# Optimization experiments

Measured on AMD Instinct MI355X. Metric: run time of the kernel, lower is better.

## Reference

```python
import jax, jax.numpy as jnp
import numpy as np

B, S, H = 16, 1024, 4
QD, KD, VD = 128, 256, 256


def setup_inputs() -> dict:
    key = jax.random.key(0)
    ks = jax.random.split(key, 12)
    s = 0.02
    return {
        "query": jax.random.normal(ks[0], (B, S, QD), jnp.float32),
        "key": jax.random.normal(ks[1], (B, S, KD), jnp.float32),
        "value": jax.random.normal(ks[2], (B, S, VD), jnp.float32),
        "Wq": jax.random.normal(ks[3], (QD, KD * H), jnp.float32) * s,
        "bq": jnp.zeros((KD * H,), jnp.float32),
        "Wk": jax.random.normal(ks[4], (KD, KD * H), jnp.float32) * s,
        "bk": jnp.zeros((KD * H,), jnp.float32),
        "Wv": jax.random.normal(ks[5], (VD, VD * H), jnp.float32) * s,
        "bv": jnp.zeros((VD * H,), jnp.float32),
        "Wo": jax.random.normal(ks[6], (VD * H, 8 * VD), jnp.float32) * s,
        "bo": jnp.zeros((8 * VD,), jnp.float32),
        "W1": jax.random.normal(ks[7], (8 * VD, 128), jnp.float32) * s,
        "b1": jnp.zeros((128,), jnp.float32),
        "random_len": S,
    }


def reference(query, key, value, Wq, bq, Wk, bk, Wv, bv, Wo, bo, W1, b1, random_len):
    b = query.shape[0]
    # flat view [B, S, H*D] -> [B, H, S, D], exactly matching torch .view semantics
    tq = (query @ Wq + bq).reshape(b, H, -1, KD)
    tk = (key @ Wk + bk).reshape(b, H, -1, KD)
    tv = (value @ Wv + bv).reshape(b, H, -1, VD)
    # NOTE: original has NO 1/sqrt(d) scaling
    scores = jnp.einsum("bhqd,bhkd->bhqk", tq, tk)  # [B,H,S,S]
    attn = jax.nn.softmax(scores, axis=-1)
    attended = jnp.einsum("bhqk,bhkd->bhqd", attn, tv)  # [B,H,S,VD]
    attended = attended.reshape(b, -1, VD * H)  # [B,S,H*VD]
    out = attended @ Wo + bo  # [B,S,2048]
    out = out.mean(axis=1)  # [B,2048]
    out = out @ W1 + b1  # [B,128]
    return out, attn
```

## Files before the change

kernel.cpp:

```cpp
#include <hip/hip_runtime.h>
#include <hip/hip_bf16.h>

typedef _Float16 half_t;
typedef _Float16 half8 __attribute__((ext_vector_type(8)));
typedef _Float16 half4v __attribute__((ext_vector_type(4)));
typedef float floatx4 __attribute__((ext_vector_type(4)));

__global__ __launch_bounds__(256) void wtrans_kernel(const float* __restrict__ W,
                                                     half_t* __restrict__ Wt, int K, int N) {
  __shared__ float sm[32][33];
  int n0 = blockIdx.x * 32, k0 = blockIdx.y * 32;
  int x = threadIdx.x & 31, y0 = threadIdx.x >> 5;
#pragma unroll
  for (int yy = 0; yy < 4; ++yy) {
    int y = y0 + yy * 8;
    sm[y][x] = W[(size_t)(k0 + y) * N + n0 + x];
  }
  __syncthreads();
#pragma unroll
  for (int yy = 0; yy < 4; ++yy) {
    int y = y0 + yy * 8;
    Wt[(size_t)(n0 + y) * K + k0 + x] = (half_t)sm[x][y];
  }
}

template <bool AF32, bool BIAS>
__global__ __launch_bounds__(256) void gemm_nt(
    const float* __restrict__ Af, const half_t* __restrict__ Ah,
    const half_t* __restrict__ Bt, const float* __restrict__ bias,
    half_t* __restrict__ C, int K, int ldc,
    size_t aStrideZ, size_t bStrideZ, size_t cStrideZ) {
  __shared__ half_t sA[128 * 32];
  __shared__ half_t sB[128 * 32];
  const int t = threadIdx.x;
  const int m0 = blockIdx.x * 128;
  const int n0 = blockIdx.y * 128;
  const int z = blockIdx.z;
  const half_t* Bz = Bt + bStrideZ * (size_t)z;
  const int w = t >> 6, lane = t & 63;
  const int wm = w & 1, wn = w >> 1;
  const int lr = lane & 15, lk = lane >> 4;
  const int srow = t >> 2, sg = t & 3;

  floatx4 acc[4][4] = {};

  for (int k0 = 0; k0 < K; k0 += 32) {
    __syncthreads();
#pragma unroll
    for (int rep = 0; rep < 2; ++rep) {
      int row = srow + rep * 64;
      int goff = (sg ^ ((row >> 1) & 3)) * 8;
      half8 hv;
      if constexpr (AF32) {
        const float* p = Af + (size_t)(m0 + row) * K + k0 + sg * 8;
        float4 f0 = *(const float4*)p;
        float4 f1 = *(const float4*)(p + 4);
        hv[0] = (half_t)f0.x; hv[1] = (half_t)f0.y;
        hv[2] = (half_t)f0.z; hv[3] = (half_t)f0.w;
        hv[4] = (half_t)f1.x; hv[5] = (half_t)f1.y;
        hv[6] = (half_t)f1.z; hv[7] = (half_t)f1.w;
      } else {
        const half_t* p = Ah + aStrideZ * (size_t)z + (size_t)(m0 + row) * K + k0 + sg * 8;
        hv = *(const half8*)p;
      }
      *(half8*)&sA[row * 32 + goff] = hv;
      const half_t* q = Bz + (size_t)(n0 + row) * K + k0 + sg * 8;
      *(half8*)&sB[row * 32 + goff] = *(const half8*)q;
    }
    __syncthreads();
    half8 af[4], bf[4];
#pragma unroll
    for (int mt = 0; mt < 4; ++mt) {
      int row = wm * 64 + mt * 16 + lr;
      af[mt] = *(const half8*)&sA[row * 32 + ((lk ^ ((row >> 1) & 3)) * 8)];
    }
#pragma unroll
    for (int nt = 0; nt < 4; ++nt) {
      int row = wn * 64 + nt * 16 + lr;
      bf[nt] = *(const half8*)&sB[row * 32 + ((lk ^ ((row >> 1) & 3)) * 8)];
    }
#pragma unroll
    for (int mt = 0; mt < 4; ++mt)
#pragma unroll
      for (int nt = 0; nt < 4; ++nt)
        acc[mt][nt] = __builtin_amdgcn_mfma_f32_16x16x32_f16(bf[nt], af[mt], acc[mt][nt], 0, 0, 0);
  }

  half_t* Cz = C + cStrideZ * (size_t)z;
#pragma unroll
  for (int mt = 0; mt < 4; ++mt) {
    int m = m0 + wm * 64 + mt * 16 + lr;
#pragma unroll
    for (int nt = 0; nt < 4; ++nt) {
      int nb = n0 + wn * 64 + nt * 16 + lk * 4;
      floatx4 a = acc[mt][nt];
      half4v h;
      if constexpr (BIAS) {
        float4 bv = *(const float4*)&bias[nb];
        h[0] = (half_t)(a[0] + bv.x); h[1] = (half_t)(a[1] + bv.y);
        h[2] = (half_t)(a[2] + bv.z); h[3] = (half_t)(a[3] + bv.w);
      } else {
        h[0] = (half_t)a[0]; h[1] = (half_t)a[1];
        h[2] = (half_t)a[2]; h[3] = (half_t)a[3];
      }
      *(half4v*)&Cz[(size_t)m * ldc + nb] = h;
    }
  }
}

__global__ __launch_bounds__(256) void softcs_kernel(float* __restrict__ attn,
                                                     float* __restrict__ cs) {
  int bh = blockIdx.x, slice = blockIdx.y;
  int t = threadIdx.x;
  int w = t >> 6, lane = t & 63;
  float csacc[16];
#pragma unroll
  for (int j = 0; j < 16; ++j) csacc[j] = 0.0f;

  for (int i = 0; i < 16; ++i) {
    int q = slice * 64 + i * 4 + w;
    float* rowp = attn + ((size_t)bh * 1024 + q) * 1024;
    const half_t* sh = (const half_t*)rowp;
    float ex[16];
    float s = 0.0f;
#pragma unroll
    for (int c = 0; c < 4; ++c) {
      half4v h = *(const half4v*)(sh + c * 256 + lane * 4);
#pragma unroll
      for (int j = 0; j < 4; ++j) {
        float e = __expf((float)h[j]);
        ex[c * 4 + j] = e;
        s += e;
      }
    }
#pragma unroll
    for (int off = 1; off < 64; off <<= 1) s += __shfl_xor(s, off);
    float rl = 1.0f / s;
#pragma unroll
    for (int c = 0; c < 4; ++c) {
      float4 o;
      o.x = ex[c * 4 + 0] * rl; o.y = ex[c * 4 + 1] * rl;
      o.z = ex[c * 4 + 2] * rl; o.w = ex[c * 4 + 3] * rl;
      *(float4*)(rowp + c * 256 + lane * 4) = o;
      csacc[c * 4 + 0] += o.x; csacc[c * 4 + 1] += o.y;
      csacc[c * 4 + 2] += o.z; csacc[c * 4 + 3] += o.w;
    }
  }
  float* csp = cs + (size_t)bh * 4096 + (size_t)w * 1024 + lane * 4;
#pragma unroll
  for (int c = 0; c < 4; ++c)
#pragma unroll
    for (int j = 0; j < 4; ++j)
      atomicAdd(csp + c * 256 + j, csacc[c * 4 + j]);
}

__global__ __launch_bounds__(256) void abar_kernel(const float* __restrict__ cs,
                                                   const half_t* __restrict__ Tv,
                                                   float* __restrict__ abar) {
  int b = blockIdx.x, r = blockIdx.y, kc = blockIdx.z;
  int d = threadIdx.x;
  __shared__ float scs[4][128];
  for (int idx = d; idx < 512; idx += 256) {
    int h = idx >> 7, k = idx & 127;
    scs[h][k] = cs[(size_t)(b * 4 + h) * 4096 + (size_t)r * 1024 + kc * 128 + k];
  }
  __syncthreads();
  float acc = 0.0f;
  for (int h = 0; h < 4; ++h) {
    const half_t* tv = Tv + (size_t)(b * 4 + h) * 262144 + (size_t)kc * 32768 + d;
#pragma unroll 4
    for (int k = 0; k < 128; ++k)
      acc += scs[h][k] * (float)tv[(size_t)k * 256];
  }
  atomicAdd(&abar[b * 1024 + r * 256 + d], acc * (1.0f / 1024.0f));
}

__global__ __launch_bounds__(256) void bcomb_kernel(const float* __restrict__ bo,
                                                    const float* __restrict__ W1,
                                                    const float* __restrict__ b1,
                                                    float* __restrict__ bcomb) {
  int t = threadIdx.x;
  int j = t & 127, h = t >> 7;
  float acc = 0.0f;
  for (int k = h * 1024; k < h * 1024 + 1024; ++k)
    acc += bo[k] * W1[(size_t)k * 128 + j];
  __shared__ float sm[2][128];
  sm[h][j] = acc;
  __syncthreads();
  if (t < 128) bcomb[t] = sm[0][t] + sm[1][t] + b1[t];
}

__global__ __launch_bounds__(256) void final2_kernel(const float* __restrict__ abar,
                                                     const half_t* __restrict__ Wcomb,
                                                     const float* __restrict__ bcomb,
                                                     float* __restrict__ out) {
  int b = blockIdx.x, t = threadIdx.x;
  int j = t & 127, h = t >> 7;
  __shared__ float sa[1024];
  __shared__ float sm[2][128];
  for (int i = t; i < 1024; i += 256) sa[i] = abar[(size_t)b * 1024 + i];
  __syncthreads();
  float acc = 0.0f;
  for (int c = h * 512; c < h * 512 + 512; ++c)
    acc += sa[c] * (float)Wcomb[(size_t)c * 128 + j];
  sm[h][j] = acc;
  __syncthreads();
  if (t < 128) out[(size_t)b * 128 + t] = sm[0][t] + sm[1][t] + bcomb[t];
}

extern "C" void kernel_launch(void* const* d_in, const int* in_sizes, int n_in,
                              void* d_out, int out_size, void* d_ws, size_t ws_size,
                              hipStream_t stream) {
  const float* query = (const float*)d_in[0];
  const float* key   = (const float*)d_in[1];
  const float* value = (const float*)d_in[2];
  const float* Wq = (const float*)d_in[3];
  const float* bq = (const float*)d_in[4];
  const float* Wk = (const float*)d_in[5];
  const float* bk = (const float*)d_in[6];
  const float* Wv = (const float*)d_in[7];
  const float* bv = (const float*)d_in[8];
  const float* Wo = (const float*)d_in[9];
  const float* bo = (const float*)d_in[10];
  const float* W1 = (const float*)d_in[11];
  const float* b1 = (const float*)d_in[12];

  char* ws = (char*)d_ws;
  half_t* Tq   = (half_t*)(ws + 0);
  half_t* Tk   = (half_t*)(ws + 33554432);
  half_t* Tv   = (half_t*)(ws + 67108864);
  float*  cs   = (float*)(ws + 100663296);
  float*  abar = (float*)(ws + 101711872);
  half_t* Wqt  = (half_t*)(ws + 101777408);
  half_t* Wkt  = (half_t*)(ws + 102039552);
  half_t* Wvt  = (half_t*)(ws + 102563840);
  half_t* W1t   = (half_t*)(ws + 0);
  half_t* Wcomb = (half_t*)(ws + 524288);
  float*  bcomb = (float*)(ws + 786432);

  float* out  = (float*)d_out;
  float* attn = out + 2048;

  hipMemsetAsync(cs, 0, 1048576 + 65536, stream);

  wtrans_kernel<<<dim3(32, 4), 256, 0, stream>>>(Wq, Wqt, 128, 1024);
  wtrans_kernel<<<dim3(32, 8), 256, 0, stream>>>(Wk, Wkt, 256, 1024);
  wtrans_kernel<<<dim3(32, 8), 256, 0, stream>>>(Wv, Wvt, 256, 1024);

  gemm_nt<true, true><<<dim3(128, 8, 1), 256, 0, stream>>>(query, nullptr, Wqt, bq, Tq, 128, 1024, 0, 0, 0);
  gemm_nt<true, true><<<dim3(128, 8, 1), 256, 0, stream>>>(key,   nullptr, Wkt, bk, Tk, 256, 1024, 0, 0, 0);
  gemm_nt<true, true><<<dim3(128, 8, 1), 256, 0, stream>>>(value, nullptr, Wvt, bv, Tv, 256, 1024, 0, 0, 0);

  gemm_nt<false, false><<<dim3(8, 8, 64), 256, 0, stream>>>(nullptr, Tq, Tk, nullptr,
      (half_t*)attn, 256, 2048, 262144, 262144, (size_t)1024 * 2048);

  wtrans_kernel<<<dim3(4, 64), 256, 0, stream>>>(W1, W1t, 2048, 128);
  gemm_nt<true, false><<<dim3(8, 1, 1), 256, 0, stream>>>(Wo, nullptr, W1t, nullptr, Wcomb, 2048, 128, 0, 0, 0);
  bcomb_kernel<<<1, 256, 0, stream>>>(bo, W1, b1, bcomb);

  softcs_kernel<<<dim3(64, 16), 256, 0, stream>>>(attn, cs);
  abar_kernel<<<dim3(16, 4, 8), 256, 0, stream>>>(cs, Tv, abar);
  final2_kernel<<<16, 256, 0, stream>>>(abar, Wcomb, bcomb, out);
}
```

Before: 733.8 us.

## Fuse QK^T score GEMM with softmax and column-sum into one kernel

Replaces the separate score GEMM, which wrote half-precision scores into the attn buffer, and the softcs pass that re-read them, with one kernel. Each block computes 32 full query rows against all 1024 keys in registers using MFMA, then applies exp, normalizes across warps through shared memory, writes fp32 attn, and atomically accumulates column sums. This removes a full round trip of the score matrix through global memory and one launch. In exchange it uses a large register footprint (32 accumulator tiles per thread) and reads the B operand straight from global memory without LDS staging, which may limit occupancy and reuse.

```diff
diff --git a/kernel.cpp b/kernel.cpp
--- a/kernel.cpp
+++ b/kernel.cpp
@@ -108,50 +108,83 @@
   }
 }
 
-__global__ __launch_bounds__(256) void softcs_kernel(float* __restrict__ attn,
-                                                     float* __restrict__ cs) {
-  int bh = blockIdx.x, slice = blockIdx.y;
-  int t = threadIdx.x;
-  int w = t >> 6, lane = t & 63;
-  float csacc[16];
-#pragma unroll
-  for (int j = 0; j < 16; ++j) csacc[j] = 0.0f;
-
-  for (int i = 0; i < 16; ++i) {
-    int q = slice * 64 + i * 4 + w;
-    float* rowp = attn + ((size_t)bh * 1024 + q) * 1024;
-    const half_t* sh = (const half_t*)rowp;
-    float ex[16];
-    float s = 0.0f;
-#pragma unroll
-    for (int c = 0; c < 4; ++c) {
-      half4v h = *(const half4v*)(sh + c * 256 + lane * 4);
-#pragma unroll
-      for (int j = 0; j < 4; ++j) {
-        float e = __expf((float)h[j]);
-        ex[c * 4 + j] = e;
-        s += e;
-      }
-    }
-#pragma unroll
-    for (int off = 1; off < 64; off <<= 1) s += __shfl_xor(s, off);
-    float rl = 1.0f / s;
-#pragma unroll
-    for (int c = 0; c < 4; ++c) {
-      float4 o;
-      o.x = ex[c * 4 + 0] * rl; o.y = ex[c * 4 + 1] * rl;
-      o.z = ex[c * 4 + 2] * rl; o.w = ex[c * 4 + 3] * rl;
-      *(float4*)(rowp + c * 256 + lane * 4) = o;
-      csacc[c * 4 + 0] += o.x; csacc[c * 4 + 1] += o.y;
-      csacc[c * 4 + 2] += o.z; csacc[c * 4 + 3] += o.w;
-    }
-  }
-  float* csp = cs + (size_t)bh * 4096 + (size_t)w * 1024 + lane * 4;
-#pragma unroll
-  for (int c = 0; c < 4; ++c)
-#pragma unroll
-    for (int j = 0; j < 4; ++j)
-      atomicAdd(csp + c * 256 + j, csacc[c * 4 + j]);
+__global__ __launch_bounds__(256, 2) void fused_attn_kernel(
+    const half_t* __restrict__ Tq, const half_t* __restrict__ Tk,
+    float* __restrict__ attn, float* __restrict__ cs) {
+  const int z = blockIdx.y;
+  const int q0 = blockIdx.x * 32;
+  const int t = threadIdx.x;
+  const int w = t >> 6, lane = t & 63;
+  const int lr = lane & 15, lk = lane >> 4;
+
+  __shared__ half_t sQ[32 * 264];
+  __shared__ float sRS[4][32];
+
+  const half_t* Tqz = Tq + (size_t)z * 262144 + (size_t)q0 * 256;
+  for (int c = t; c < 1024; c += 256) {
+    int row = c >> 5, col8 = (c & 31) * 8;
+    *(half8*)&sQ[row * 264 + col8] = *(const half8*)&Tqz[row * 256 + col8];
+  }
+  __syncthreads();
+
+  const half_t* Tkz = Tk + (size_t)z * 262144;
+  const int nb = w * 256;
+
+  floatx4 acc[2][16] = {};
+  for (int k0 = 0; k0 < 256; k0 += 32) {
+    half8 af0 = *(const half8*)&sQ[lr * 264 + k0 + lk * 8];
+    half8 af1 = *(const half8*)&sQ[(16 + lr) * 264 + k0 + lk * 8];
+#pragma unroll
+    for (int nt = 0; nt < 16; ++nt) {
+      half8 bf = *(const half8*)&Tkz[(size_t)(nb + nt * 16 + lr) * 256 + k0 + lk * 8];
+      acc[0][nt] = __builtin_amdgcn_mfma_f32_16x16x32_f16(bf, af0, acc[0][nt], 0, 0, 0);
+      acc[1][nt] = __builtin_amdgcn_mfma_f32_16x16x32_f16(bf, af1, acc[1][nt], 0, 0, 0);
+    }
+  }
+
+  float rs0 = 0.0f, rs1 = 0.0f;
+#pragma unroll
+  for (int nt = 0; nt < 16; ++nt) {
+#pragma unroll
+    for (int j = 0; j < 4; ++j) {
+      float v0 = __expf(acc[0][nt][j]);
+      float v1 = __expf(acc[1][nt][j]);
+      acc[0][nt][j] = v0; acc[1][nt][j] = v1;
+      rs0 += v0; rs1 += v1;
+    }
+  }
+  rs0 += __shfl_xor(rs0, 16); rs0 += __shfl_xor(rs0, 32);
+  rs1 += __shfl_xor(rs1, 16); rs1 += __shfl_xor(rs1, 32);
+  if (lane < 16) { sRS[w][lane] = rs0; sRS[w][16 + lane] = rs1; }
+  __syncthreads();
+  float inv0 = 1.0f / (sRS[0][lr] + sRS[1][lr] + sRS[2][lr] + sRS[3][lr]);
+  float inv1 = 1.0f / (sRS[0][16 + lr] + sRS[1][16 + lr] + sRS[2][16 + lr] + sRS[3][16 + lr]);
+
+  float* attnz = attn + (size_t)z * 1048576;
+  float* csz = cs + (size_t)z * 4096;
+#pragma unroll
+  for (int nt = 0; nt < 16; ++nt) {
+    int n = nb + nt * 16 + lk * 4;
+    float4 o0, o1;
+    o0.x = acc[0][nt][0] * inv0; o0.y = acc[0][nt][1] * inv0;
+    o0.z = acc[0][nt][2] * inv0; o0.w = acc[0][nt][3] * inv0;
+    o1.x = acc[1][nt][0] * inv1; o1.y = acc[1][nt][1] * inv1;
+    o1.z = acc[1][nt][2] * inv1; o1.w = acc[1][nt][3] * inv1;
+    *(float4*)&attnz[(size_t)(q0 + lr) * 1024 + n] = o0;
+    *(float4*)&attnz[(size_t)(q0 + 16 + lr) * 1024 + n] = o1;
+    float c0 = o0.x + o1.x, c1 = o0.y + o1.y, c2 = o0.z + o1.z, c3 = o0.w + o1.w;
+    c0 += __shfl_xor(c0, 4); c0 += __shfl_xor(c0, 8);
+    c1 += __shfl_xor(c1, 4); c1 += __shfl_xor(c1, 8);
+    c2 += __shfl_xor(c2, 4); c2 += __shfl_xor(c2, 8);
+    c3 += __shfl_xor(c3, 4); c3 += __shfl_xor(c3, 8);
+    if (lr < 4) {
+      float* p = csz + (size_t)lr * 1024 + n;
+      atomicAdd(p + 0, c0);
+      atomicAdd(p + 1, c1);
+      atomicAdd(p + 2, c2);
+      atomicAdd(p + 3, c3);
+    }
+  }
 }
 
 __global__ __launch_bounds__(256) void abar_kernel(const float* __restrict__ cs,
@@ -251,14 +284,12 @@
   gemm_nt<true, true><<<dim3(128, 8, 1), 256, 0, stream>>>(key,   nullptr, Wkt, bk, Tk, 256, 1024, 0, 0, 0);
   gemm_nt<true, true><<<dim3(128, 8, 1), 256, 0, stream>>>(value, nullptr, Wvt, bv, Tv, 256, 1024, 0, 0, 0);
 
-  gemm_nt<false, false><<<dim3(8, 8, 64), 256, 0, stream>>>(nullptr, Tq, Tk, nullptr,
-      (half_t*)attn, 256, 2048, 262144, 262144, (size_t)1024 * 2048);
+  fused_attn_kernel<<<dim3(32, 64), 256, 0, stream>>>(Tq, Tk, attn, cs);
 
   wtrans_kernel<<<dim3(4, 64), 256, 0, stream>>>(W1, W1t, 2048, 128);
   gemm_nt<true, false><<<dim3(8, 1, 1), 256, 0, stream>>>(Wo, nullptr, W1t, nullptr, Wcomb, 2048, 128, 0, 0, 0);
   bcomb_kernel<<<1, 256, 0, stream>>>(bo, W1, b1, bcomb);
 
-  softcs_kernel<<<dim3(64, 16), 256, 0, stream>>>(attn, cs);
   abar_kernel<<<dim3(16, 4, 8), 256, 0, stream>>>(cs, Tv, abar);
   final2_kernel<<<16, 256, 0, stream>>>(abar, Wcomb, bcomb, out);
 }
```

Measured after the change: 808.5 us. 1.1x slower.
